# Kernel optimization log

Measured on AMD Instinct MI355X. Metric: run time of the kernel, lower is better.

## Reference

```python
import jax, jax.numpy as jnp
import numpy as np


def setup_inputs() -> dict:
    key = jax.random.key(0)
    k1, k2, k3, k4 = jax.random.split(key, 4)
    bs, ch, T = 8, 256, 512
    N, P = 2048, 16
    feat = jax.random.normal(k1, (bs, ch, T), dtype=jnp.float32)
    # rois: [N, 3] = (batch_idx, start, end) in feature coordinates
    bidx = jax.random.randint(k2, (N,), 0, bs).astype(jnp.float32)
    u1 = jax.random.uniform(k3, (N,), dtype=jnp.float32)
    u2 = jax.random.uniform(k4, (N,), dtype=jnp.float32)
    start = u1 * (T - 1)
    end = start + u2 * (T - start)
    rois = jnp.stack([bidx, start, end], axis=1).astype(jnp.float32)
    return {"input": feat, "rois": rois, "feature_dim": P, "ratio": 4}


def reference(input, rois, feature_dim, ratio):
    # 1D ROI Align: input [bs, ch, T], rois [N, 3]=(batch_idx, start, end)
    # -> output [N, ch, feature_dim]
    bs, ch, T = input.shape
    bidx = rois[:, 0].astype(jnp.int32)              # [N]
    start = rois[:, 1]
    end = rois[:, 2]
    roi_len = jnp.maximum(end - start, 1.0)          # malformed ROI guard
    bin_size = roi_len / feature_dim                 # [N]
    S = ratio                                        # samples per bin (static)
    p = jnp.arange(feature_dim, dtype=jnp.float32)   # bin index
    s = (jnp.arange(S, dtype=jnp.float32) + 0.5) / S # fractional offset in bin
    # sample coordinates x: [N, P, S]
    x = start[:, None, None] + (p[None, :, None] + s[None, None, :]) * bin_size[:, None, None]
    valid = (x >= -1.0) & (x <= T)                   # out-of-range samples -> 0
    xc = jnp.clip(x, 0.0, T - 1)
    x_low = jnp.floor(xc).astype(jnp.int32)
    x_high = jnp.minimum(x_low + 1, T - 1)
    lx = xc - x_low.astype(jnp.float32)              # linear interp weight
    b = bidx[:, None, None]                          # [N,1,1]
    v_low = input[b, :, x_low]                       # [N, P, S, ch]
    v_high = input[b, :, x_high]                     # [N, P, S, ch]
    val = v_low * (1.0 - lx[..., None]) + v_high * lx[..., None]
    val = jnp.where(valid[..., None], val, 0.0)
    out = val.mean(axis=2)                           # average over samples -> [N, P, ch]
    return jnp.transpose(out, (0, 2, 1))             # [N, ch, P]
```

## Files before the change

### kernel.cpp

```cpp
#include <hip/hip_runtime.h>


#define T_DIM 512
#define CH    256
#define P_DIM 16
#define S_RAT 4
#define CTILE 8
#define NCT   (CH / CTILE)
#define RSPLIT 4
#define MAXSL  512
#define MAXMETA 160

typedef _Float16 h2 __attribute__((ext_vector_type(2)));

__device__ __forceinline__ float dot2_acc(h2 a, h2 b, float c) {
#if __has_builtin(__builtin_amdgcn_fdot2)
    return __builtin_amdgcn_fdot2(a, b, c, false);
#else
    return fmaf((float)a.x, (float)b.x, fmaf((float)a.y, (float)b.y, c));
#endif
}

__device__ __forceinline__ unsigned pack2(float a, float b) {
    union { h2 h; unsigned u; } u;
    u.h = h2{(_Float16)a, (_Float16)b};
    return u.u;
}

__global__ __launch_bounds__(256) void roialign_lds_kernel(
    const float* __restrict__ feat,
    const float* __restrict__ rois,
    float* __restrict__ out,
    int N)
{
    __shared__ __align__(16) uint4 tile[2 * T_DIM];
    __shared__ float4 s_meta[MAXMETA];
    __shared__ int    s_cnt;

    const int ct  = blockIdx.x;
    const int r   = blockIdx.y;
    const int b   = blockIdx.z;
    const int tid = threadIdx.x;

    const int q = tid >> 7;
    const int k = tid & 127;
    float4 v0, v1, v2, v3;
    float  n0, n1, n2, n3;
    {
        const float* base = feat + ((size_t)b * CH + ct * CTILE + 4 * q) * T_DIM;
        const int nidx = (4 * k + 4 < T_DIM) ? (4 * k + 4) : (T_DIM - 1);
        v0 = ((const float4*)(base + 0 * T_DIM))[k];  n0 = (base + 0 * T_DIM)[nidx];
        v1 = ((const float4*)(base + 1 * T_DIM))[k];  n1 = (base + 1 * T_DIM)[nidx];
        v2 = ((const float4*)(base + 2 * T_DIM))[k];  n2 = (base + 2 * T_DIM)[nidx];
        v3 = ((const float4*)(base + 3 * T_DIM))[k];  n3 = (base + 3 * T_DIM)[nidx];
    }

    if (tid == 0) s_cnt = 0;
    asm volatile("s_waitcnt lgkmcnt(0)" ::: "memory");
    __builtin_amdgcn_s_barrier();
    asm volatile("" ::: "memory");

    {
        const int lane = tid & 63;
#pragma unroll
        for (int h = 0; h < MAXSL / 256; ++h) {
            const int i = r * MAXSL + h * 256 + tid;
            bool match = false;
            float sx = 0.0f, ex = 0.0f;
            if (i < N) {
                float bf = rois[3 * i];
                sx = rois[3 * i + 1];
                ex = rois[3 * i + 2];
                match = ((int)bf == b);
            }
            unsigned long long mask = __ballot(match);
            const int pre = __popcll(mask & ((1ull << lane) - 1ull));
            const int tot = __popcll(mask);
            int wbase = 0;
            if (lane == 0 && tot) wbase = atomicAdd(&s_cnt, tot);
            wbase = __shfl(wbase, 0);
            if (match) {
                const int pos = wbase + pre;
                if (pos < MAXMETA)
                    s_meta[pos] = make_float4((float)i, sx, ex, 0.0f);
            }
        }
    }

    {
        uint4* trow = &tile[q * T_DIM];
        trow[0 * 128 + k] = make_uint4(pack2(v0.x, v0.y), pack2(v1.x, v1.y),
                                       pack2(v2.x, v2.y), pack2(v3.x, v3.y));
        trow[1 * 128 + k] = make_uint4(pack2(v0.y, v0.z), pack2(v1.y, v1.z),
                                       pack2(v2.y, v2.z), pack2(v3.y, v3.z));
        trow[2 * 128 + k] = make_uint4(pack2(v0.z, v0.w), pack2(v1.z, v1.w),
                                       pack2(v2.z, v2.w), pack2(v3.z, v3.w));
        trow[3 * 128 + k] = make_uint4(pack2(v0.w, n0), pack2(v1.w, n1),
                                       pack2(v2.w, n2), pack2(v3.w, n3));
    }
    __syncthreads();
    const int cnt = min(s_cnt, MAXMETA);

    const int rs = tid >> 4;
    const int p  = tid & 15;

    float qf[S_RAT];
#pragma unroll
    for (int s = 0; s < S_RAT; ++s)
        qf[s] = (float)p + ((float)s + 0.5f) * (1.0f / S_RAT);

    const char* tbase = (const char*)tile;

    for (int base2 = 0; base2 < cnt; base2 += 16) {
        const int i = base2 + rs;
        if (i >= cnt) break;

        const float4 m     = s_meta[i];
        const float  start = m.y;
        const float  bin   = fmaxf(m.z - start, 1.0f) * (1.0f / P_DIM);

        int boff[S_RAT];
        h2  wp[S_RAT];
#pragma unroll
        for (int s = 0; s < S_RAT; ++s) {
            float x  = fmaf(qf[s], bin, start);
            float xc = fminf(x, (float)(T_DIM - 1));
            float tf = fminf(truncf(xc), (float)(T_DIM - 2));
            const int t = (int)tf;
            const float w = xc - tf;
            wp[s]   = h2{(_Float16)((1.0f - w) * (1.0f / S_RAT)),
                         (_Float16)(w * (1.0f / S_RAT))};
            boff[s] = ((t & 3) << 11) | ((t >> 2) << 4);
        }

        float* outn = out + (size_t)(int)m.x * (CH * P_DIM) + ct * (CTILE * P_DIM) + p;
#pragma unroll
        for (int qq = 0; qq < 2; ++qq) {
            float a0 = 0.0f, a1 = 0.0f, a2 = 0.0f, a3 = 0.0f;
#pragma unroll
            for (int s = 0; s < S_RAT; ++s) {
                const uint4 e = *(const uint4*)(tbase + qq * 8192 + boff[s]);
                union { unsigned u; h2 h; } c0, c1, c2, c3;
                c0.u = e.x; c1.u = e.y; c2.u = e.z; c3.u = e.w;
                a0 = dot2_acc(c0.h, wp[s], a0);
                a1 = dot2_acc(c1.h, wp[s], a1);
                a2 = dot2_acc(c2.h, wp[s], a2);
                a3 = dot2_acc(c3.h, wp[s], a3);
            }
            outn[(4 * qq + 0) * P_DIM] = a0;
            outn[(4 * qq + 1) * P_DIM] = a1;
            outn[(4 * qq + 2) * P_DIM] = a2;
            outn[(4 * qq + 3) * P_DIM] = a3;
        }
    }
}

extern "C" void kernel_launch(void* const* d_in, const int* in_sizes, int n_in,
                              void* d_out, int out_size, void* d_ws, size_t ws_size,
                              hipStream_t stream) {
    const float* feat = (const float*)d_in[0];
    const float* rois = (const float*)d_in[1];
    float* out = (float*)d_out;
    const int N = in_sizes[1] / 3;

    dim3 grid(NCT, RSPLIT, 8);
    roialign_lds_kernel<<<grid, dim3(256), 0, stream>>>(feat, rois, out, N);
}
```

Before: 74.85 us.

## Double ROI split per block and replace LDS atomics with wave-prefix compaction

Each block now scans 256 ROIs instead of 512, which doubles the grid along the ROI axis (8 splits) and shrinks the metadata buffer. ROI compaction now uses per-wave ballot counts written to LDS and a prefix sum, replacing the atomicAdd loop, and the ROI loads are issued early alongside the feature loads. More blocks means more parallelism and less serial ROI work per block, but each feature tile is now loaded and converted twice as often. MAXMETA drops to 96, which is enough only if no batch holds more than 96 ROIs in a 256-ROI slice.

```diff
diff --git a/kernel.cpp b/kernel.cpp
--- a/kernel.cpp
+++ b/kernel.cpp
@@ -7,9 +7,9 @@
 #define S_RAT 4
 #define CTILE 8
 #define NCT   (CH / CTILE)
-#define RSPLIT 4
-#define MAXSL  512
-#define MAXMETA 160
+#define RSPLIT 8
+#define MAXSL  256
+#define MAXMETA 96
 
 typedef _Float16 h2 __attribute__((ext_vector_type(2)));
 
@@ -35,12 +35,23 @@
 {
     __shared__ __align__(16) uint4 tile[2 * T_DIM];
     __shared__ float4 s_meta[MAXMETA];
-    __shared__ int    s_cnt;
+    __shared__ int    s_wcnt[4];
+    __shared__ int    s_tot;
 
     const int ct  = blockIdx.x;
     const int r   = blockIdx.y;
     const int b   = blockIdx.z;
     const int tid = threadIdx.x;
+    const int wv  = tid >> 6;
+    const int lane = tid & 63;
+
+    const int ri = r * MAXSL + tid;
+    float bf = -1.0f, sx = 0.0f, ex = 0.0f;
+    if (ri < N) {
+        bf = rois[3 * ri];
+        sx = rois[3 * ri + 1];
+        ex = rois[3 * ri + 2];
+    }
 
     const int q = tid >> 7;
     const int k = tid & 127;
@@ -55,35 +66,24 @@
         v3 = ((const float4*)(base + 3 * T_DIM))[k];  n3 = (base + 3 * T_DIM)[nidx];
     }
 
-    if (tid == 0) s_cnt = 0;
-    asm volatile("s_waitcnt lgkmcnt(0)" ::: "memory");
-    __builtin_amdgcn_s_barrier();
-    asm volatile("" ::: "memory");
+    const bool match = (ri < N) && ((int)bf == b);
+    {
+        unsigned long long mask = __ballot(match);
+        const int tot = __popcll(mask);
+        if (lane == 0) s_wcnt[wv] = tot;
+        const int pre = __popcll(mask & ((1ull << lane) - 1ull));
 
-    {
-        const int lane = tid & 63;
-#pragma unroll
-        for (int h = 0; h < MAXSL / 256; ++h) {
-            const int i = r * MAXSL + h * 256 + tid;
-            bool match = false;
-            float sx = 0.0f, ex = 0.0f;
-            if (i < N) {
-                float bf = rois[3 * i];
-                sx = rois[3 * i + 1];
-                ex = rois[3 * i + 2];
-                match = ((int)bf == b);
-            }
-            unsigned long long mask = __ballot(match);
-            const int pre = __popcll(mask & ((1ull << lane) - 1ull));
-            const int tot = __popcll(mask);
-            int wbase = 0;
-            if (lane == 0 && tot) wbase = atomicAdd(&s_cnt, tot);
-            wbase = __shfl(wbase, 0);
-            if (match) {
-                const int pos = wbase + pre;
-                if (pos < MAXMETA)
-                    s_meta[pos] = make_float4((float)i, sx, ex, 0.0f);
-            }
+        asm volatile("s_waitcnt lgkmcnt(0)" ::: "memory");
+        __builtin_amdgcn_s_barrier();
+        asm volatile("" ::: "memory");
+
+        const int c0 = s_wcnt[0], c1 = s_wcnt[1], c2 = s_wcnt[2], c3 = s_wcnt[3];
+        if (tid == 0) s_tot = c0 + c1 + c2 + c3;
+        const int wbase = (wv > 0 ? c0 : 0) + (wv > 1 ? c1 : 0) + (wv > 2 ? c2 : 0);
+        if (match) {
+            const int pos = wbase + pre;
+            if (pos < MAXMETA)
+                s_meta[pos] = make_float4((float)ri, sx, ex, 0.0f);
         }
     }
 
@@ -99,7 +99,7 @@
                                        pack2(v2.w, n2), pack2(v3.w, n3));
     }
     __syncthreads();
-    const int cnt = min(s_cnt, MAXMETA);
+    const int cnt = min(s_tot, MAXMETA);
 
     const int rs = tid >> 4;
     const int p  = tid & 15;
```

Result: no change. 74.92 us (+0.1%).
